# Kernel optimization log

Hardware: AMD Instinct MI355X
Metric: run time of the kernel (lower is better)

Reference implementation:

```python
import jax, jax.numpy as jnp
import numpy as np

B, NCLASS, NSUPP = 4096, 1000, 64
NCHUNK = NSUPP * NSUPP  # 4096, x's feature dim


def setup_inputs() -> dict:
    key = jax.random.key(0)
    k1, k2, k3 = jax.random.split(key, 3)
    x = jax.random.normal(k1, (B, NCHUNK), dtype=jnp.float32)
    # torch .uniform_(-1, 1)
    wSupp = jax.random.uniform(k2, (NCLASS, NSUPP), dtype=jnp.float32, minval=-1.0, maxval=1.0)
    chunk_map = jax.random.randint(k3, (NCLASS, NSUPP), 0, NCHUNK, dtype=jnp.int32)
    return {"x": x, "wSupp": wSupp, "chunk_map": chunk_map}


def reference(x, wSupp, chunk_map):
    # sparse_support: for each class i, feat_i = sum_j x[:, chunk_map[i,j]] * wSupp[i,j]; out = exp(feat)
    gathered = x[:, chunk_map]                      # [B, nClass, nSupp] gather via index map
    feats = jnp.einsum('bcs,cs->bc', gathered, wSupp)  # weighted sum over support
    return jnp.exp(feats)                           # [B, nClass]
```

## Files before the change

kernel.cpp:

```cpp
#include <hip/hip_runtime.h>
#include <hip/hip_fp16.h>


constexpr int B_       = 4096;
constexpr int NCLASS_  = 1000;
constexpr int NSUPP_   = 64;
constexpr int NCHUNK_  = 4096;
constexpr int BT       = 8;
constexpr int THREADS_ = 1024;
constexpr int SG_      = NSUPP_ / 4;
constexpr size_t CMT_BYTES = (size_t)SG_ * NCLASS_ * 16;
constexpr size_t WS_NEEDED = 2 * CMT_BYTES;

__global__ __launch_bounds__(256)
void build_cw_kernel(const int*   __restrict__ cm,
                     const float* __restrict__ w,
                     int*         __restrict__ cmT,
                     float*       __restrict__ wT)
{
    const int t    = threadIdx.x;
    const int c    = blockIdx.x * 4 + (t >> 6);
    const int lane = t & 63;
    if (c >= NCLASS_) return;

    const int   idx = cm[c * NSUPP_ + lane];
    const float wv  = w [c * NSUPP_ + lane];
    const int   key = (idx - c) & 7;

    const unsigned long long below = ((unsigned long long)1 << lane) - 1;
    int j = 0;
    #pragma unroll
    for (int r = 0; r < 8; ++r) {
        const unsigned long long m = __ballot(key == r);
        const int cnt = __popcll(m);
        if (key > r)  j += cnt;
        if (key == r) j += __popcll(m & below);
    }

    const int dst = ((j >> 2) * NCLASS_ + c) * 4 + (j & 3);
    cmT[dst] = idx;
    wT [dst] = wv;
}

template <bool USET>
__global__ __launch_bounds__(THREADS_, 8)
void supp_gather_kernel(const float* __restrict__ x,
                        const float* __restrict__ wSupp,
                        const int*   __restrict__ cmap,
                        const float4* __restrict__ wT,
                        const int4*   __restrict__ cmT,
                        float*       __restrict__ out)
{
    __shared__ __align__(16) __half2 tile[NCHUNK_ * (BT / 2)];

    const int t  = threadIdx.x;
    const int rb = blockIdx.x * BT;

    #pragma unroll
    for (int p = 0; p < NCHUNK_ / THREADS_; ++p) {
        const int col = t + THREADS_ * p;
        float v[BT];
        #pragma unroll
        for (int bi = 0; bi < BT; ++bi)
            v[bi] = x[(size_t)(rb + bi) * NCHUNK_ + col];
        __half2 h[BT / 2];
        #pragma unroll
        for (int k = 0; k < BT / 2; ++k)
            h[k] = __floats2half2_rn(v[2 * k], v[2 * k + 1]);
        *reinterpret_cast<float4*>(&tile[(size_t)col * 4]) =
            *reinterpret_cast<float4*>(h);
    }
    __syncthreads();

    if (t < NCLASS_) {
        const int c = t;
        const float4* tile4 = reinterpret_cast<const float4*>(tile);
        float acc[BT] = {0.f, 0.f, 0.f, 0.f, 0.f, 0.f, 0.f, 0.f};

        int4   ci;
        float4 wf;
        if constexpr (USET) { ci = cmT[c];               wf = wT[c]; }
        else {
            ci = reinterpret_cast<const int4*>(cmap + c * NSUPP_)[0];
            wf = reinterpret_cast<const float4*>(wSupp + c * NSUPP_)[0];
        }

        for (int sg = 0; sg < SG_; ++sg) {
            float4 d0 = tile4[ci.x];
            float4 d1 = tile4[ci.y];
            float4 d2 = tile4[ci.z];
            float4 d3 = tile4[ci.w];
            const float4 wv = wf;

            const int sgn = (sg + 1 < SG_) ? sg + 1 : SG_ - 1;
            if constexpr (USET) {
                ci = cmT[sgn * NCLASS_ + c];
                wf = wT [sgn * NCLASS_ + c];
            } else {
                ci = reinterpret_cast<const int4*>(cmap + c * NSUPP_)[sgn];
                wf = reinterpret_cast<const float4*>(wSupp + c * NSUPP_)[sgn];
            }

            const float4* dp[4] = {&d0, &d1, &d2, &d3};
            const float   ws4[4] = {wv.x, wv.y, wv.z, wv.w};
            #pragma unroll
            for (int j = 0; j < 4; ++j) {
                const __half2* h2 = reinterpret_cast<const __half2*>(dp[j]);
                #pragma unroll
                for (int k = 0; k < 4; ++k) {
                    const float2 f = __half22float2(h2[k]);
                    acc[2 * k]     = fmaf(f.x, ws4[j], acc[2 * k]);
                    acc[2 * k + 1] = fmaf(f.y, ws4[j], acc[2 * k + 1]);
                }
            }
        }
        #pragma unroll
        for (int bi = 0; bi < BT; ++bi)
            out[(size_t)(rb + bi) * NCLASS_ + c] = __expf(acc[bi]);
    }
}

extern "C" void kernel_launch(void* const* d_in, const int* in_sizes, int n_in,
                              void* d_out, int out_size, void* d_ws, size_t ws_size,
                              hipStream_t stream) {
    const float* x  = (const float*)d_in[0];
    const float* w  = (const float*)d_in[1];
    const int*   cm = (const int*)d_in[2];
    float*       o  = (float*)d_out;

    int*   cmT = (int*)d_ws;
    float* wT  = (float*)((char*)d_ws + CMT_BYTES);

    const dim3 grid(B_ / BT);
    if (ws_size >= WS_NEEDED) {
        build_cw_kernel<<<dim3((NCLASS_ + 3) / 4), dim3(256), 0, stream>>>(
            cm, w, cmT, wT);
        supp_gather_kernel<true><<<grid, dim3(THREADS_), 0, stream>>>(
            x, w, cm, (const float4*)wT, (const int4*)cmT, o);
    } else {
        supp_gather_kernel<false><<<grid, dim3(THREADS_), 0, stream>>>(
            x, w, cm, (const float4*)wT, (const int4*)cmT, o);
    }
}
```

Measured before the change: 115.7 us.

## Double batch rows per block to sixteen and reuse each gathered index

Result: no change. 115.0 us (-0.6%).

```diff
diff --git a/kernel.cpp b/kernel.cpp
--- a/kernel.cpp
+++ b/kernel.cpp
@@ -6,7 +6,7 @@
 constexpr int NCLASS_  = 1000;
 constexpr int NSUPP_   = 64;
 constexpr int NCHUNK_  = 4096;
-constexpr int BT       = 8;
+constexpr int BT       = 16;
 constexpr int THREADS_ = 1024;
 constexpr int SG_      = NSUPP_ / 4;
 constexpr size_t CMT_BYTES = (size_t)SG_ * NCLASS_ * 16;
@@ -25,15 +25,14 @@
 
     const int   idx = cm[c * NSUPP_ + lane];
     const float wv  = w [c * NSUPP_ + lane];
-    const int   key = (idx - c) & 7;
+    const int   key = (idx - c) & 3;
 
     const unsigned long long below = ((unsigned long long)1 << lane) - 1;
     int j = 0;
     #pragma unroll
-    for (int r = 0; r < 8; ++r) {
+    for (int r = 0; r < 4; ++r) {
         const unsigned long long m = __ballot(key == r);
-        const int cnt = __popcll(m);
-        if (key > r)  j += cnt;
+        if (key > r)  j += __popcll(m);
         if (key == r) j += __popcll(m & below);
     }
 
@@ -43,7 +42,7 @@
 }
 
 template <bool USET>
-__global__ __launch_bounds__(THREADS_, 8)
+__global__ __launch_bounds__(THREADS_, 4)
 void supp_gather_kernel(const float* __restrict__ x,
                         const float* __restrict__ wSupp,
                         const int*   __restrict__ cmap,
@@ -56,6 +55,16 @@
     const int t  = threadIdx.x;
     const int rb = blockIdx.x * BT;
 
+    int4   ci;
+    float4 wf;
+    if (t < NCLASS_) {
+        if constexpr (USET) { ci = cmT[t]; wf = wT[t]; }
+        else {
+            ci = reinterpret_cast<const int4*>(cmap + t * NSUPP_)[0];
+            wf = reinterpret_cast<const float4*>(wSupp + t * NSUPP_)[0];
+        }
+    }
+
     #pragma unroll
     for (int p = 0; p < NCHUNK_ / THREADS_; ++p) {
         const int col = t + THREADS_ * p;
@@ -67,29 +76,25 @@
         #pragma unroll
         for (int k = 0; k < BT / 2; ++k)
             h[k] = __floats2half2_rn(v[2 * k], v[2 * k + 1]);
-        *reinterpret_cast<float4*>(&tile[(size_t)col * 4]) =
-            *reinterpret_cast<float4*>(h);
+        *reinterpret_cast<float4*>(&tile[(size_t)col * 8]) =
+            *reinterpret_cast<float4*>(&h[0]);
+        *reinterpret_cast<float4*>(&tile[(size_t)col * 8 + 4]) =
+            *reinterpret_cast<float4*>(&h[4]);
     }
     __syncthreads();
 
     if (t < NCLASS_) {
         const int c = t;
         const float4* tile4 = reinterpret_cast<const float4*>(tile);
-        float acc[BT] = {0.f, 0.f, 0.f, 0.f, 0.f, 0.f, 0.f, 0.f};
-
-        int4   ci;
-        float4 wf;
-        if constexpr (USET) { ci = cmT[c];               wf = wT[c]; }
-        else {
-            ci = reinterpret_cast<const int4*>(cmap + c * NSUPP_)[0];
-            wf = reinterpret_cast<const float4*>(wSupp + c * NSUPP_)[0];
-        }
+        float acc[BT];
+        #pragma unroll
+        for (int bi = 0; bi < BT; ++bi) acc[bi] = 0.f;
 
         for (int sg = 0; sg < SG_; ++sg) {
-            float4 d0 = tile4[ci.x];
-            float4 d1 = tile4[ci.y];
-            float4 d2 = tile4[ci.z];
-            float4 d3 = tile4[ci.w];
+            float4 d0a = tile4[2 * ci.x],     d0b = tile4[2 * ci.x + 1];
+            float4 d1a = tile4[2 * ci.y],     d1b = tile4[2 * ci.y + 1];
+            float4 d2a = tile4[2 * ci.z],     d2b = tile4[2 * ci.z + 1];
+            float4 d3a = tile4[2 * ci.w],     d3b = tile4[2 * ci.w + 1];
             const float4 wv = wf;
 
             const int sgn = (sg + 1 < SG_) ? sg + 1 : SG_ - 1;
@@ -101,16 +106,21 @@
                 wf = reinterpret_cast<const float4*>(wSupp + c * NSUPP_)[sgn];
             }
 
-            const float4* dp[4] = {&d0, &d1, &d2, &d3};
+            const float4* dpa[4] = {&d0a, &d1a, &d2a, &d3a};
+            const float4* dpb[4] = {&d0b, &d1b, &d2b, &d3b};
             const float   ws4[4] = {wv.x, wv.y, wv.z, wv.w};
             #pragma unroll
             for (int j = 0; j < 4; ++j) {
-                const __half2* h2 = reinterpret_cast<const __half2*>(dp[j]);
+                const __half2* ha = reinterpret_cast<const __half2*>(dpa[j]);
+                const __half2* hb = reinterpret_cast<const __half2*>(dpb[j]);
                 #pragma unroll
                 for (int k = 0; k < 4; ++k) {
-                    const float2 f = __half22float2(h2[k]);
-                    acc[2 * k]     = fmaf(f.x, ws4[j], acc[2 * k]);
-                    acc[2 * k + 1] = fmaf(f.y, ws4[j], acc[2 * k + 1]);
+                    const float2 fa = __half22float2(ha[k]);
+                    const float2 fb = __half22float2(hb[k]);
+                    acc[2 * k]      = fmaf(fa.x, ws4[j], acc[2 * k]);
+                    acc[2 * k + 1]  = fmaf(fa.y, ws4[j], acc[2 * k + 1]);
+                    acc[8 + 2 * k]     = fmaf(fb.x, ws4[j], acc[8 + 2 * k]);
+                    acc[8 + 2 * k + 1] = fmaf(fb.y, ws4[j], acc[8 + 2 * k + 1]);
                 }
             }
         }
```
